# Optimization experiments

Measured on AMD Instinct MI355X. Metric: run time of the kernel, lower is better.

Reference implementation:

```python
import jax, jax.numpy as jnp
import numpy as np


def _avgpool2(x):
    # 2x2 average pool, stride 2 (NCHW)
    n, c, h, w = x.shape
    return x.reshape(n, c, h // 2, 2, w // 2, 2).mean(axis=(3, 5))


def setup_inputs() -> dict:
    key = jax.random.key(0)
    k1, k2, k3, k4 = jax.random.split(key, 4)
    N, H, W = 32, 512, 512
    N2 = H // 4
    eps = 1e-4  # keep probabilities strictly inside (0,1) for BCE
    logits = jax.random.uniform(k1, (N, 1, H, W), jnp.float32, eps, 1.0 - eps)
    labels = jax.random.uniform(k2, (N, 1, H, W), jnp.float32, eps, 1.0 - eps)
    v_attention = jax.random.uniform(k3, (N, 1, N2, N2), jnp.float32)
    h_attention = jax.random.uniform(k4, (N, 1, N2, N2), jnp.float32)
    return {"logits": logits, "labels": labels,
            "v_attention": v_attention, "h_attention": h_attention}


def reference(logits, labels, v_attention, h_attention):
    N = labels.shape[0]
    smooth = 1.0

    # --- BCE over all elements ---
    p = logits.reshape(-1)
    y = labels.reshape(-1)
    bceloss = -jnp.mean(y * jnp.log(p) + (1.0 - y) * jnp.log(1.0 - p))

    # --- Dice on thresholded logits ---
    masks = (logits > 0.4).astype(logits.dtype)
    input_flat = masks.reshape(N, -1)
    target_flat = labels.reshape(N, -1)
    intersection = (input_flat * target_flat).sum(axis=1)
    dice = 2.0 * (intersection + smooth) / (input_flat.sum(axis=1) + target_flat.sum(axis=1) + smooth)
    diceloss = 1.0 - dice.sum() / N

    # --- Per-sample 3-way Pearson-style correlation ---
    N1 = v_attention.shape[0]
    attent_labels = _avgpool2(_avgpool2(labels))          # [N,1,H/4,W/4]
    v = v_attention.reshape(N1, -1)                        # [N1, N2*N2]
    h = h_attention.reshape(N1, -1)
    l = attent_labels.reshape(N1, -1)
    vc = v - v.mean(axis=1, keepdims=True)
    hc = h - h.mean(axis=1, keepdims=True)
    lc = l - l.mean(axis=1, keepdims=True)
    num = (vc * hc * lc).sum(axis=1)
    den = jnp.sqrt((vc * vc).sum(axis=1) * (hc * hc).sum(axis=1) * (lc * lc).sum(axis=1))
    cor_loss = -(num / den).sum() / N1

    return 0.2 * bceloss + 0.3 * diceloss + 0.5 * cor_loss
```

## Files before the change

### kernel.cpp

```cpp
#include <hip/hip_runtime.h>
#include <math.h>

#define NSAMP 32
#define HW 512
#define PW 128
#define NPOOL (PW * PW)
#define BPS 16
#define NBLOCKS (NSAMP * BPS)
#define PPT 4
#define NACC 14

typedef float f32x4 __attribute__((ext_vector_type(4)));

__device__ __forceinline__ void gload2x4(f32x4& r0, f32x4& r1, const float* p) {
    asm volatile("global_load_dwordx4 %0, %2, off\n\t"
                 "global_load_dwordx4 %1, %2, off offset:2048"
                 : "=v"(r0), "=v"(r1) : "v"(p) : "memory");
}
__device__ __forceinline__ void gload4(float& a, float& b, float& c, float& d,
                                       const float* p) {
    asm volatile("global_load_dword %0, %4, off\n\t"
                 "global_load_dword %1, %4, off offset:1024\n\t"
                 "global_load_dword %2, %4, off offset:2048\n\t"
                 "global_load_dword %3, %4, off offset:3072"
                 : "=v"(a), "=v"(b), "=v"(c), "=v"(d) : "v"(p) : "memory");
}

#define WAITV(n)  do { asm volatile("s_waitcnt vmcnt(" #n ")" ::: "memory"); \
                       __builtin_amdgcn_sched_barrier(0); } while (0)

__device__ __forceinline__ float wave_sum_dpp(float x) {
#define DPP_ADD(ctrl)                                                         \
    x += __int_as_float(__builtin_amdgcn_update_dpp(                          \
        0, __float_as_int(x), (ctrl), 0xf, 0xf, true));
    DPP_ADD(0x111)
    DPP_ADD(0x112)
    DPP_ADD(0x114)
    DPP_ADD(0x118)
    DPP_ADD(0x142)
    DPP_ADD(0x143)
#undef DPP_ADD
    return x;
}

__global__ __launch_bounds__(256) void covloss_main(
    const float* __restrict__ logits, const float* __restrict__ labels,
    const float* __restrict__ v_att,  const float* __restrict__ h_att,
    float* __restrict__ part)
{
    const int bid   = blockIdx.x;
    const int n     = bid >> 4;
    const int local = bid & 15;
    const int pbase = local * (PPT * 256);
    const int tid   = threadIdx.x;

    const float* lg = logits + (size_t)n * HW * HW;
    const float* lb = labels + (size_t)n * HW * HW;

    float bce = 0.f, inter = 0.f, ysum = 0.f;
    unsigned long long cnt_u = 0;
    float S_v = 0.f, S_h = 0.f, S_l = 0.f;
    float S_vv = 0.f, S_hh = 0.f, S_ll = 0.f;
    float S_vh = 0.f, S_vl = 0.f, S_hl = 0.f, S_vhl = 0.f;

    f32x4 LA0, LA1, LA2, LA3, YA0, YA1, YA2, YA3;
    f32x4 LB0, LB1, LB2, LB3, YB0, YB1, YB2, YB3;
    float v0, v1, v2, v3, h0, h1, h2, h3;

#define STAGE(S, p) do {                                                      \
    const int pidx = pbase + (p) * 256 + tid;                                 \
    const int pr = pidx >> 7, pc = pidx & 127;                                \
    const float* baL = lg + (size_t)(4 * pr) * HW + 4 * pc;                   \
    const float* baY = lb + (size_t)(4 * pr) * HW + 4 * pc;                   \
    gload2x4(L##S##0, L##S##1, baL);                                          \
    gload2x4(L##S##2, L##S##3, baL + 2 * HW);                                 \
    gload2x4(Y##S##0, Y##S##1, baY);                                          \
    gload2x4(Y##S##2, Y##S##3, baY + 2 * HW);                                 \
} while (0)

#define ROW(Lr, Yr) do {                                                      \
    _Pragma("unroll")                                                         \
    for (int j = 0; j < 4; ++j) {                                             \
        const float pp = (Lr)[j], y = (Yr)[j];                                \
        bce = fmaf(y, __log2f(pp), bce);                                      \
        bce = fmaf(1.f - y, __log2f(1.f - pp), bce);                          \
        const bool m = pp > 0.4f;                                             \
        cnt_u += __popcll(__ballot(m));                                       \
        inter += m ? y : 0.f;                                                 \
        lsum  += y;                                                           \
    }                                                                         \
} while (0)

#define COMPUTE(S, vS, hS) do {                                               \
    float lsum = 0.f;                                                         \
    ROW(L##S##0, Y##S##0); ROW(L##S##1, Y##S##1);                             \
    ROW(L##S##2, Y##S##2); ROW(L##S##3, Y##S##3);                             \
    ysum += lsum;                                                             \
    const float l = lsum * 0.0625f;                                           \
    S_v += vS; S_h += hS; S_l += l;                                           \
    S_vv = fmaf(vS, vS, S_vv); S_hh = fmaf(hS, hS, S_hh);                     \
    S_ll = fmaf(l, l, S_ll);                                                  \
    const float vh = vS * hS;                                                 \
    S_vh += vh; S_vl = fmaf(vS, l, S_vl); S_hl = fmaf(hS, l, S_hl);           \
    S_vhl = fmaf(vh, l, S_vhl);                                               \
} while (0)

    gload4(v0, v1, v2, v3, v_att + (size_t)n * NPOOL + pbase + tid);
    gload4(h0, h1, h2, h3, h_att + (size_t)n * NPOOL + pbase + tid);
    STAGE(A, 0);
    STAGE(B, 1);

    WAITV(8);
    COMPUTE(A, v0, h0);
    STAGE(A, 2);
    WAITV(8);
    COMPUTE(B, v1, h1);
    STAGE(B, 3);
    WAITV(8);
    COMPUTE(A, v2, h2);
    WAITV(0);
    COMPUTE(B, v3, h3);

#undef STAGE
#undef ROW
#undef COMPUTE

    float vals[13] = { bce, inter, ysum,
                       S_v, S_h, S_l, S_vv, S_hh, S_ll,
                       S_vh, S_vl, S_hl, S_vhl };
#pragma unroll
    for (int k = 0; k < 13; ++k) vals[k] = wave_sum_dpp(vals[k]);

    __shared__ float sh[4][NACC];
    const int lane = tid & 63, wv = tid >> 6;
    if (lane == 63) {
        sh[wv][0] = vals[0];
        sh[wv][1] = (float)cnt_u;
        sh[wv][2] = vals[1];
        sh[wv][3] = vals[2];
#pragma unroll
        for (int k = 3; k < 13; ++k) sh[wv][k + 1] = vals[k];
    }
    __syncthreads();
    if (tid < NACC) {
        part[(size_t)tid * NBLOCKS + bid] =
            sh[0][tid] + sh[1][tid] + sh[2][tid] + sh[3][tid];
    }
}

__global__ __launch_bounds__(256) void covloss_finalize(
    const float* __restrict__ part, float* __restrict__ out)
{
    const int t = threadIdx.x;
    __shared__ double acc[NSAMP][NACC];

    for (int pair = t; pair < NSAMP * NACC; pair += 256) {
        const int s = pair / NACC, k = pair % NACC;
        const float4* p = (const float4*)(part + (size_t)k * NBLOCKS + s * BPS);
        double a = 0.0;
#pragma unroll
        for (int i = 0; i < 4; ++i) {
            const float4 q = p[i];
            a += (double)q.x + (double)q.y + (double)q.z + (double)q.w;
        }
        acc[s][k] = a;
    }
    __syncthreads();

    __shared__ double sb[NSAMP], sd[NSAMP], sc[NSAMP];
    if (t < NSAMP) {
        const double* a = acc[t];
        const double nn = (double)NPOOL;
        const double cvv = a[7] - a[4] * a[4] / nn;
        const double chh = a[8] - a[5] * a[5] / nn;
        const double cll = a[9] - a[6] * a[6] / nn;
        const double num = a[13]
            - (a[4] * a[12] + a[5] * a[11] + a[6] * a[10]) / nn
            + 2.0 * a[4] * a[5] * a[6] / (nn * nn);
        sc[t] = num / sqrt(cvv * chh * cll);
        sd[t] = 2.0 * (a[2] + 1.0) / (a[1] + a[3] + 1.0);
        sb[t] = a[0];
    }
    __syncthreads();
    if (t == 0) {
        double bces = 0.0, ds = 0.0, cs = 0.0;
#pragma unroll
        for (int i = 0; i < NSAMP; ++i) { bces += sb[i]; ds += sd[i]; cs += sc[i]; }
        const double bceloss = -(bces * M_LN2) / ((double)NSAMP * HW * HW);
        out[0] = (float)(0.2 * bceloss + 0.3 * (1.0 - ds / NSAMP) + 0.5 * (-cs / NSAMP));
    }
}

extern "C" void kernel_launch(void* const* d_in, const int* in_sizes, int n_in,
                              void* d_out, int out_size, void* d_ws, size_t ws_size,
                              hipStream_t stream) {
    const float* logits = (const float*)d_in[0];
    const float* labels = (const float*)d_in[1];
    const float* v_att  = (const float*)d_in[2];
    const float* h_att  = (const float*)d_in[3];
    float* out  = (float*)d_out;
    float* part = (float*)d_ws;

    covloss_main<<<NBLOCKS, 256, 0, stream>>>(logits, labels, v_att, h_att, part);
    covloss_finalize<<<1, 256, 0, stream>>>(part, out);
}
```

Measured before the change: 20.43 us.

## Fuse finalize into main kernel via last-block atomic counters

Removes the separate finalize kernel launch. Each block publishes its partial sums and bumps a per-sample counter, and the last block for a sample reduces that sample's partials and writes per-sample results. A global counter then selects the last sample-finisher to produce the final scalar. The counters are monotonic, with baselines read at block start, so no reset is needed between calls. This saves a launch gap at the cost of atomics, and it relies on relaxed atomics plus vmcnt waits for ordering, with no explicit release/acquire fences.

```diff
diff --git a/kernel.cpp b/kernel.cpp
--- a/kernel.cpp
+++ b/kernel.cpp
@@ -11,6 +11,29 @@
 #define NACC 14
 
 typedef float f32x4 __attribute__((ext_vector_type(4)));
+typedef unsigned long long u64;
+
+
+__device__ __forceinline__ float agloadf(const float* p) {
+    return __hip_atomic_load(p, __ATOMIC_RELAXED, __HIP_MEMORY_SCOPE_AGENT);
+}
+__device__ __forceinline__ void agstoref(float* p, float v) {
+    __hip_atomic_store(p, v, __ATOMIC_RELAXED, __HIP_MEMORY_SCOPE_AGENT);
+}
+__device__ __forceinline__ double agloadd(const double* p) {
+    u64 u = __hip_atomic_load((const u64*)p, __ATOMIC_RELAXED, __HIP_MEMORY_SCOPE_AGENT);
+    return __longlong_as_double((long long)u);
+}
+__device__ __forceinline__ void agstored(double* p, double v) {
+    __hip_atomic_store((u64*)p, (u64)__double_as_longlong(v),
+                       __ATOMIC_RELAXED, __HIP_MEMORY_SCOPE_AGENT);
+}
+__device__ __forceinline__ u64 agloadu(const u64* p) {
+    return __hip_atomic_load(p, __ATOMIC_RELAXED, __HIP_MEMORY_SCOPE_AGENT);
+}
+__device__ __forceinline__ u64 agbump(u64* p) {
+    return __hip_atomic_fetch_add(p, 1ULL, __ATOMIC_RELAXED, __HIP_MEMORY_SCOPE_AGENT);
+}
 
 __device__ __forceinline__ void gload2x4(f32x4& r0, f32x4& r1, const float* p) {
     asm volatile("global_load_dwordx4 %0, %2, off\n\t"
@@ -43,16 +66,24 @@
     return x;
 }
 
-__global__ __launch_bounds__(256) void covloss_main(
+__global__ __launch_bounds__(256) void covloss_fused(
     const float* __restrict__ logits, const float* __restrict__ labels,
     const float* __restrict__ v_att,  const float* __restrict__ h_att,
-    float* __restrict__ part)
+    float* __restrict__ out, u64* __restrict__ ws)
 {
     const int bid   = blockIdx.x;
     const int n     = bid >> 4;
     const int local = bid & 15;
     const int pbase = local * (PPT * 256);
     const int tid   = threadIdx.x;
+
+    u64*    cnt_s = (u64*)((char*)ws + 64 * n);
+    u64*    cnt_f = (u64*)((char*)ws + 2048);
+    float*  part  = (float*)((char*)ws + 4096);
+    double* res   = (double*)((char*)ws + 36864);
+
+    u64 s0 = 0, f0 = 0;
+    if (tid == 0) { s0 = agloadu(cnt_s); f0 = agloadu(cnt_f); }
 
     const float* lg = logits + (size_t)n * HW * HW;
     const float* lb = labels + (size_t)n * HW * HW;
@@ -142,34 +173,34 @@
         for (int k = 3; k < 13; ++k) sh[wv][k + 1] = vals[k];
     }
     __syncthreads();
+
     if (tid < NACC) {
-        part[(size_t)tid * NBLOCKS + bid] =
-            sh[0][tid] + sh[1][tid] + sh[2][tid] + sh[3][tid];
-    }
-}
-
-__global__ __launch_bounds__(256) void covloss_finalize(
-    const float* __restrict__ part, float* __restrict__ out)
-{
-    const int t = threadIdx.x;
-    __shared__ double acc[NSAMP][NACC];
-
-    for (int pair = t; pair < NSAMP * NACC; pair += 256) {
-        const int s = pair / NACC, k = pair % NACC;
-        const float4* p = (const float4*)(part + (size_t)k * NBLOCKS + s * BPS);
+        const float p = sh[0][tid] + sh[1][tid] + sh[2][tid] + sh[3][tid];
+        agstoref(&part[(size_t)tid * NBLOCKS + bid], p);
+    }
+
+    __shared__ int sampWin;
+    if (tid == 0) {
+        WAITV(0);
+        const u64 old = agbump(cnt_s);
+        sampWin = (old == s0 + (BPS - 1));
+    }
+    __syncthreads();
+    if (!sampWin) return;
+
+    __shared__ double accd[NACC];
+    if (tid < NACC) {
+        const float* p = part + (size_t)tid * NBLOCKS + n * BPS;
         double a = 0.0;
 #pragma unroll
-        for (int i = 0; i < 4; ++i) {
-            const float4 q = p[i];
-            a += (double)q.x + (double)q.y + (double)q.z + (double)q.w;
-        }
-        acc[s][k] = a;
-    }
-    __syncthreads();
-
-    __shared__ double sb[NSAMP], sd[NSAMP], sc[NSAMP];
-    if (t < NSAMP) {
-        const double* a = acc[t];
+        for (int i = 0; i < BPS; ++i) a += (double)agloadf(p + i);
+        accd[tid] = a;
+    }
+    __syncthreads();
+
+    __shared__ int finWin;
+    if (tid == 0) {
+        const double* a = accd;
         const double nn = (double)NPOOL;
         const double cvv = a[7] - a[4] * a[4] / nn;
         const double chh = a[8] - a[5] * a[5] / nn;
@@ -177,15 +208,27 @@
         const double num = a[13]
             - (a[4] * a[12] + a[5] * a[11] + a[6] * a[10]) / nn
             + 2.0 * a[4] * a[5] * a[6] / (nn * nn);
-        sc[t] = num / sqrt(cvv * chh * cll);
-        sd[t] = 2.0 * (a[2] + 1.0) / (a[1] + a[3] + 1.0);
-        sb[t] = a[0];
-    }
-    __syncthreads();
-    if (t == 0) {
+        agstored(&res[n * 3 + 0], a[0]);
+        agstored(&res[n * 3 + 1], 2.0 * (a[2] + 1.0) / (a[1] + a[3] + 1.0));
+        agstored(&res[n * 3 + 2], num / sqrt(cvv * chh * cll));
+        WAITV(0);
+        const u64 old2 = agbump(cnt_f);
+        finWin = (old2 == f0 + (NSAMP - 1));
+    }
+    __syncthreads();
+    if (!finWin) return;
+
+    __shared__ double rb[NSAMP], rd[NSAMP], rc[NSAMP];
+    if (tid < NSAMP) {
+        rb[tid] = agloadd(&res[tid * 3 + 0]);
+        rd[tid] = agloadd(&res[tid * 3 + 1]);
+        rc[tid] = agloadd(&res[tid * 3 + 2]);
+    }
+    __syncthreads();
+    if (tid == 0) {
         double bces = 0.0, ds = 0.0, cs = 0.0;
 #pragma unroll
-        for (int i = 0; i < NSAMP; ++i) { bces += sb[i]; ds += sd[i]; cs += sc[i]; }
+        for (int i = 0; i < NSAMP; ++i) { bces += rb[i]; ds += rd[i]; cs += rc[i]; }
         const double bceloss = -(bces * M_LN2) / ((double)NSAMP * HW * HW);
         out[0] = (float)(0.2 * bceloss + 0.3 * (1.0 - ds / NSAMP) + 0.5 * (-cs / NSAMP));
     }
@@ -198,9 +241,8 @@
     const float* labels = (const float*)d_in[1];
     const float* v_att  = (const float*)d_in[2];
     const float* h_att  = (const float*)d_in[3];
-    float* out  = (float*)d_out;
-    float* part = (float*)d_ws;
-
-    covloss_main<<<NBLOCKS, 256, 0, stream>>>(logits, labels, v_att, h_att, part);
-    covloss_finalize<<<1, 256, 0, stream>>>(part, out);
-}
+    float* out = (float*)d_out;
+    u64*   ws  = (u64*)d_ws;
+
+    covloss_fused<<<NBLOCKS, 256, 0, stream>>>(logits, labels, v_att, h_att, out, ws);
+}
```

Result: slower. 21.47 us (+5.1%).
